# Optimization experiments

Measured on AMD Instinct MI355X. Metric: run time of the kernel, lower is better.

Reference implementation:

```python
import jax, jax.numpy as jnp
import numpy as np

HIDDEN = 512
HEADS = 8
LN_EPS = 1e-5


def setup_inputs() -> dict:
    key = jax.random.key(0)
    ks = jax.random.split(key, 10)
    n, bsz, h = 128, 4, HIDDEN
    state = jax.random.normal(ks[0], (n, n, bsz, h), dtype=jnp.float32)
    relation = jax.random.normal(ks[1], (n, n, bsz, h), dtype=jnp.float32)
    attn_mask = jnp.zeros((n, bsz, n), dtype=bool)  # key_padding_mask, True = pad
    std = 0.02
    Wq = jax.random.normal(ks[2], (h, h), dtype=jnp.float32) * std
    bq = jnp.zeros((h,), dtype=jnp.float32)
    Wk = jax.random.normal(ks[3], (h, h), dtype=jnp.float32) * std
    bk = jnp.zeros((h,), dtype=jnp.float32)
    Wp = jax.random.normal(ks[4], (h, 2 * h), dtype=jnp.float32) * std
    bp = jnp.zeros((h,), dtype=jnp.float32)
    gamma = jnp.ones((h,), dtype=jnp.float32)
    beta = jnp.zeros((h,), dtype=jnp.float32)
    return {"state": state, "relation": relation, "attn_mask": attn_mask, "n": n,
            "Wq": Wq, "bq": bq, "Wk": Wk, "bk": bk, "Wp": Wp, "bp": bp,
            "gamma": gamma, "beta": beta}


def reference(state, relation, attn_mask, n, Wq, bq, Wk, bk, Wp, bp, gamma, beta):
    # state, relation: [n, n, bsz, h]; attn_mask: [n, bsz, n] (True = pad key)
    h = state.shape[-1]
    dh = h // HEADS
    scale = dh ** -0.5
    # per-row self-attention weights (eval mode: attention dropout is identity)
    q = (jnp.einsum('itbh,oh->itbo', state, Wq) + bq) * scale
    k = jnp.einsum('isbh,oh->isbo', state, Wk) + bk
    qh = q.reshape(q.shape[0], q.shape[1], q.shape[2], HEADS, dh)
    kh = k.reshape(k.shape[0], k.shape[1], k.shape[2], HEADS, dh)
    scores = jnp.einsum('itbnd,isbnd->ibnts', qh, kh)  # [n, bsz, H, t, s]
    pad = attn_mask[:, :, None, None, :]               # [n, bsz, 1, 1, s]
    scores = jnp.where(pad, -jnp.inf, scores)
    probs = jax.nn.softmax(scores, axis=-1)
    w = probs.mean(axis=2)                             # avg over heads -> [n, bsz, t, s]
    # x[i,t,b] = sum_s w[i,b,t,s] * state[i,s,b]
    x = jnp.einsum('ibts,isbh->itbh', w, state)
    # rel_mix[i,t,b] = sum_s w[i,b,t,s] * relation[s,t,b]
    rel_mix = jnp.einsum('ibts,stbh->itbh', w, relation)
    cat = jnp.concatenate([x, rel_mix], axis=-1)       # [n, n, bsz, 2h]
    out = jax.nn.relu(jnp.einsum('itbc,hc->itbh', cat, Wp) + bp)
    # dropout is identity in eval mode; residual + layernorm
    y = state + out
    mu = y.mean(axis=-1, keepdims=True)
    var = y.var(axis=-1, keepdims=True)
    return gamma * (y - mu) * jax.lax.rsqrt(var + LN_EPS) + beta
```

## Files before the change

kernel.cpp:

```cpp
#include <hip/hip_runtime.h>

typedef unsigned short u16;
typedef __attribute__((ext_vector_type(4))) unsigned short u16x4;
typedef __attribute__((ext_vector_type(8))) unsigned short u16x8;
typedef __attribute__((ext_vector_type(8))) short bf16x8;
typedef __attribute__((ext_vector_type(4))) float f32x4;

__device__ __forceinline__ u16 f2bf(float f) {
  union { float f; unsigned u; } v; v.f = f;
  unsigned r = v.u + 0x7fffu + ((v.u >> 16) & 1u);
  return (u16)(r >> 16);
}
__device__ __forceinline__ float bf2f(u16 u) {
  union { unsigned u; float f; } v; v.u = ((unsigned)u) << 16;
  return v.f;
}
__device__ __forceinline__ u16x8 pack8(f32x4 a, f32x4 b) {
  u16x8 r = { f2bf(a.x), f2bf(a.y), f2bf(a.z), f2bf(a.w),
              f2bf(b.x), f2bf(b.y), f2bf(b.z), f2bf(b.w) };
  return r;
}
__device__ __forceinline__ void gload16(const void* g, void* l) {
  __builtin_amdgcn_global_load_lds(
      (const __attribute__((address_space(1))) unsigned int*)g,
      (__attribute__((address_space(3))) unsigned int*)l, 16, 0, 0);
}

__global__ __launch_bounds__(256) void k_prep(
    const float* __restrict__ Wq, const float* __restrict__ Wk,
    const float* __restrict__ bq, const float* __restrict__ bk,
    const float* __restrict__ Wp,
    u16* __restrict__ wqk, u16* __restrict__ wp, float* __restrict__ bqk) {
  int idx = blockIdx.x * 256 + threadIdx.x;
  if (idx < 524288) {
    int o = idx >> 9, hh = idx & 511;
    wqk[idx] = f2bf((o < 512) ? Wq[o * 512 + hh] * 0.125f : Wk[(o - 512) * 512 + hh]);
    wp[idx] = f2bf(Wp[idx]);
  }
  if (idx < 1024) bqk[idx] = (idx < 512) ? bq[idx] * 0.125f : bk[idx - 512];
}

__global__ __launch_bounds__(256) void k_cast(
    const float* __restrict__ src, u16* __restrict__ dst) {
  size_t idx = ((size_t)blockIdx.x * 256 + threadIdx.x) * 8;
  f32x4 v0 = *(const f32x4*)&src[idx];
  f32x4 v1 = *(const f32x4*)&src[idx + 4];
  *(u16x8*)&dst[idx] = pack8(v0, v1);
}

__global__ __launch_bounds__(256) void k_qkproj(
    const u16* __restrict__ stB, const u16* __restrict__ wqk,
    const float* __restrict__ bqk, u16* __restrict__ qk) {
  const int flat = blockIdx.x;
  const int xcd = flat & 7, local = flat >> 3;
  const int m0 = (xcd * 64 + (local >> 3)) * 128;
  const int n0 = (local & 7) * 128;
  __shared__ u16 smem[17408];
  u16* As = smem;
  u16* Bs = smem + 8192;
  const int tid = threadIdx.x, lane = tid & 63, wid = tid >> 6;
  const int l15 = lane & 15, l4 = lane >> 4;
  const int wm = (wid >> 1) * 64, wn = (wid & 1) * 64;
  const int lr = lane >> 3;
  const int lcs = ((lane & 7) ^ lr) * 8;
  const int s7 = l15 & 7;
  const f32x4 fz = {0.f, 0.f, 0.f, 0.f};
  f32x4 acc[4][4];
#pragma unroll
  for (int a = 0; a < 4; ++a)
#pragma unroll
    for (int c = 0; c < 4; ++c) acc[a][c] = fz;
  for (int k0 = 0; k0 < 512; k0 += 64) {
    if (k0) __syncthreads();
#pragma unroll
    for (int j = 0; j < 4; ++j) {
      int rb = wid * 32 + j * 8;
      gload16(&stB[(size_t)(m0 + rb + lr) * 512 + k0 + lcs], &As[rb * 64]);
      gload16(&wqk[(size_t)(n0 + rb + lr) * 512 + k0 + lcs], &Bs[rb * 64]);
    }
    __syncthreads();
#pragma unroll
    for (int kk = 0; kk < 64; kk += 32) {
      const int cshift = (((kk >> 3) + l4) ^ s7) * 8;
      bf16x8 af[4], bfr[4];
#pragma unroll
      for (int mf = 0; mf < 4; ++mf)
        af[mf] = *(const bf16x8*)&As[(wm + mf * 16 + l15) * 64 + cshift];
#pragma unroll
      for (int nf = 0; nf < 4; ++nf)
        bfr[nf] = *(const bf16x8*)&Bs[(wn + nf * 16 + l15) * 64 + cshift];
#pragma unroll
      for (int mf = 0; mf < 4; ++mf)
#pragma unroll
        for (int nf = 0; nf < 4; ++nf)
          acc[mf][nf] = __builtin_amdgcn_mfma_f32_16x16x32_bf16(af[mf], bfr[nf], acc[mf][nf], 0, 0, 0);
    }
  }
  float bias[4];
#pragma unroll
  for (int nf = 0; nf < 4; ++nf) bias[nf] = bqk[n0 + wn + nf * 16 + l15];
  __syncthreads();
  u16* Cs = smem;
#pragma unroll
  for (int mf = 0; mf < 4; ++mf)
#pragma unroll
    for (int nf = 0; nf < 4; ++nf)
#pragma unroll
      for (int r = 0; r < 4; ++r)
        Cs[(wm + mf * 16 + l4 * 4 + r) * 136 + wn + nf * 16 + l15] =
            f2bf(acc[mf][nf][r] + bias[nf]);
  __syncthreads();
#pragma unroll
  for (int rr = 0; rr < 8; ++rr) {
    int row = rr * 16 + (tid >> 4), c8 = (tid & 15) * 8;
    *(u16x8*)&qk[(size_t)(m0 + row) * 1024 + n0 + c8] = *(const u16x8*)&Cs[row * 136 + c8];
  }
}

__global__ __launch_bounds__(512) void k_scores(
    const u16* __restrict__ qk, const unsigned char* __restrict__ mask,
    u16* __restrict__ wbuf) {
  const int i = blockIdx.x, b = blockIdx.y;
  __shared__ u16 smem[2 * 128 * 72];
  u16* qs = smem;
  u16* ks = smem + 128 * 72;
  const int tid = threadIdx.x, lane = tid & 63, wid = tid >> 6;
  const int l15 = lane & 15, l4 = lane >> 4;
  float wacc[8][4];
#pragma unroll
  for (int nf = 0; nf < 8; ++nf)
#pragma unroll
    for (int r = 0; r < 4; ++r) wacc[nf][r] = 0.f;
  bool mk[8];
#pragma unroll
  for (int nf = 0; nf < 8; ++nf) mk[nf] = mask[i * 512 + b * 128 + nf * 16 + l15] != 0;
  const int arow = tid >> 3, acol = (tid & 7) * 8;
  const f32x4 fz = {0.f, 0.f, 0.f, 0.f};
  for (int h = 0; h < 8; ++h) {
    __syncthreads();
#pragma unroll
    for (int rr = 0; rr < 2; ++rr) {
      int row = rr * 64 + arow;
      int base = ((i * 128 + row) * 4 + b) * 1024 + h * 64 + acol;
      *(u16x8*)&qs[row * 72 + acol] = *(const u16x8*)&qk[base];
      *(u16x8*)&ks[row * 72 + acol] = *(const u16x8*)&qk[base + 512];
    }
    __syncthreads();
    f32x4 sc[8];
#pragma unroll
    for (int nf = 0; nf < 8; ++nf) sc[nf] = fz;
#pragma unroll
    for (int kk = 0; kk < 64; kk += 32) {
      bf16x8 a = *(const bf16x8*)&qs[(wid * 16 + l15) * 72 + kk + l4 * 8];
#pragma unroll
      for (int nf = 0; nf < 8; ++nf) {
        bf16x8 bb = *(const bf16x8*)&ks[(nf * 16 + l15) * 72 + kk + l4 * 8];
        sc[nf] = __builtin_amdgcn_mfma_f32_16x16x32_bf16(a, bb, sc[nf], 0, 0, 0);
      }
    }
#pragma unroll
    for (int r = 0; r < 4; ++r) {
      float mx = -3e38f;
#pragma unroll
      for (int nf = 0; nf < 8; ++nf) mx = fmaxf(mx, mk[nf] ? -3e38f : sc[nf][r]);
#pragma unroll
      for (int d = 1; d < 16; d <<= 1) mx = fmaxf(mx, __shfl_xor(mx, d, 64));
      float p[8], sum = 0.f;
#pragma unroll
      for (int nf = 0; nf < 8; ++nf) {
        p[nf] = mk[nf] ? 0.f : __expf(sc[nf][r] - mx);
        sum += p[nf];
      }
#pragma unroll
      for (int d = 1; d < 16; d <<= 1) sum += __shfl_xor(sum, d, 64);
      float inv = 0.125f / sum;
#pragma unroll
      for (int nf = 0; nf < 8; ++nf) wacc[nf][r] += p[nf] * inv;
    }
  }
#pragma unroll
  for (int nf = 0; nf < 8; ++nf)
#pragma unroll
    for (int r = 0; r < 4; ++r) {
      int t = wid * 16 + l4 * 4 + r;
      wbuf[((i * 4 + b) * 128 + t) * 128 + nf * 16 + l15] = f2bf(wacc[nf][r]);
    }
}

__global__ __launch_bounds__(256) void k_mix(
    const u16* __restrict__ stB, const float* __restrict__ relation,
    const u16* __restrict__ wbuf, u16* __restrict__ xbuf, u16* __restrict__ relbuf) {
  const int q = blockIdx.x, b = blockIdx.y;
  const int hc = blockIdx.z & 3, path = blockIdx.z >> 2;
  __shared__ u16 smem[2 * 128 * 136];
  u16* AT = smem;
  u16* WS = smem + 128 * 136;
  u16* T = WS;
  const int tid = threadIdx.x, lane = tid & 63, wid = tid >> 6;
  const int l15 = lane & 15, l4 = lane >> 4;
  const int wh = (wid >> 1) * 64, wc = (wid & 1) * 64;
  const int sr = tid >> 3, hseg = (tid & 7) * 16;
  const int th = tid >> 1, sseg = (tid & 1) * 16;
#pragma unroll
  for (int ch = 0; ch < 4; ++ch) {
    const int sbase = ch * 32;
    u16x8 r0, r1;
    if (path == 0) {
      size_t gaddr = ((size_t)(q * 128 + sbase + sr) * 4 + b) * 512 + hc * 128 + hseg;
      r0 = *(const u16x8*)&stB[gaddr];
      r1 = *(const u16x8*)&stB[gaddr + 8];
    } else {
      size_t gaddr = (((size_t)(sbase + sr) * 128 + q) * 4 + b) * 512 + hc * 128 + hseg;
      f32x4 v0 = *(const f32x4*)&relation[gaddr];
      f32x4 v1 = *(const f32x4*)&relation[gaddr + 4];
      f32x4 v2 = *(const f32x4*)&relation[gaddr + 8];
      f32x4 v3 = *(const f32x4*)&relation[gaddr + 12];
      r0 = pack8(v0, v1);
      r1 = pack8(v2, v3);
    }
    __syncthreads();
    *(u16x8*)&T[sr * 136 + hseg] = r0;
    *(u16x8*)&T[sr * 136 + hseg + 8] = r1;
    __syncthreads();
    u16x8 c0, c1;
#pragma unroll
    for (int j = 0; j < 8; ++j) c0[j] = T[(sseg + j) * 136 + th];
#pragma unroll
    for (int j = 0; j < 8; ++j) c1[j] = T[(sseg + 8 + j) * 136 + th];
    *(u16x8*)&AT[th * 136 + sbase + sseg] = c0;
    *(u16x8*)&AT[th * 136 + sbase + sseg + 8] = c1;
  }
  __syncthreads();
  const int r16 = tid >> 4, c8 = (tid & 15) * 8;
#pragma unroll
  for (int rr = 0; rr < 8; ++rr) {
    int row = rr * 16 + r16;
    const u16* src = (path == 0) ? &wbuf[((q * 4 + b) * 128 + row) * 128 + c8]
                                 : &wbuf[((row * 4 + b) * 128 + q) * 128 + c8];
    *(u16x8*)&WS[row * 136 + c8] = *(const u16x8*)src;
  }
  __syncthreads();
  const f32x4 fz = {0.f, 0.f, 0.f, 0.f};
  f32x4 acc[4][4];
#pragma unroll
  for (int a = 0; a < 4; ++a)
#pragma unroll
    for (int c = 0; c < 4; ++c) acc[a][c] = fz;
#pragma unroll
  for (int kk = 0; kk < 128; kk += 32) {
    bf16x8 af[4], bfr[4];
#pragma unroll
    for (int mf = 0; mf < 4; ++mf)
      af[mf] = *(const bf16x8*)&AT[(wh + mf * 16 + l15) * 136 + kk + l4 * 8];
#pragma unroll
    for (int nf = 0; nf < 4; ++nf)
      bfr[nf] = *(const bf16x8*)&WS[(wc + nf * 16 + l15) * 136 + kk + l4 * 8];
#pragma unroll
    for (int mf = 0; mf < 4; ++mf)
#pragma unroll
      for (int nf = 0; nf < 4; ++nf)
        acc[mf][nf] = __builtin_amdgcn_mfma_f32_16x16x32_bf16(af[mf], bfr[nf], acc[mf][nf], 0, 0, 0);
  }
  __syncthreads();
  u16* Cs = smem;
#pragma unroll
  for (int mf = 0; mf < 4; ++mf)
#pragma unroll
    for (int nf = 0; nf < 4; ++nf) {
      int h0 = wh + mf * 16 + l4 * 4;
      int oc = wc + nf * 16 + l15;
      u16x4 pk = { f2bf(acc[mf][nf][0]), f2bf(acc[mf][nf][1]),
                   f2bf(acc[mf][nf][2]), f2bf(acc[mf][nf][3]) };
      *(u16x4*)&Cs[oc * 136 + h0] = pk;
    }
  __syncthreads();
#pragma unroll
  for (int rr = 0; rr < 8; ++rr) {
    int o = rr * 16 + r16;
    u16x8 v = *(const u16x8*)&Cs[o * 136 + c8];
    if (path == 0)
      *(u16x8*)&xbuf[((q * 128 + o) * 4 + b) * 512 + hc * 128 + c8] = v;
    else
      *(u16x8*)&relbuf[((o * 128 + q) * 4 + b) * 512 + hc * 128 + c8] = v;
  }
}

__global__ __launch_bounds__(256) void k_proj(
    const u16* __restrict__ xbuf, const u16* __restrict__ relbuf,
    const u16* __restrict__ wp, const float* __restrict__ bp,
    u16* __restrict__ yb) {
  const int flat = blockIdx.x;
  const int xcd = flat & 7, local = flat >> 3;
  const int m0 = (xcd * 64 + (local >> 2)) * 128;
  const int n0 = (local & 3) * 128;
  __shared__ u16 smem[17408];
  u16* As = smem;
  u16* Bs = smem + 8192;
  const int tid = threadIdx.x, lane = tid & 63, wid = tid >> 6;
  const int l15 = lane & 15, l4 = lane >> 4;
  const int wm = (wid >> 1) * 64, wn = (wid & 1) * 64;
  const int lr = lane >> 3;
  const int lcs = ((lane & 7) ^ lr) * 8;
  const int s7 = l15 & 7;
  const f32x4 fz = {0.f, 0.f, 0.f, 0.f};
  f32x4 acc[4][4];
#pragma unroll
  for (int a = 0; a < 4; ++a)
#pragma unroll
    for (int c = 0; c < 4; ++c) acc[a][c] = fz;
  for (int k0 = 0; k0 < 1024; k0 += 64) {
    if (k0) __syncthreads();
    const u16* abase = (k0 < 512) ? xbuf + k0 : relbuf + (k0 - 512);
#pragma unroll
    for (int j = 0; j < 4; ++j) {
      int rb = wid * 32 + j * 8;
      gload16(&abase[(size_t)(m0 + rb + lr) * 512 + lcs], &As[rb * 64]);
      gload16(&wp[(size_t)(n0 + rb + lr) * 1024 + k0 + lcs], &Bs[rb * 64]);
    }
    __syncthreads();
#pragma unroll
    for (int kk = 0; kk < 64; kk += 32) {
      const int cshift = (((kk >> 3) + l4) ^ s7) * 8;
      bf16x8 af[4], bfr[4];
#pragma unroll
      for (int mf = 0; mf < 4; ++mf)
        af[mf] = *(const bf16x8*)&As[(wm + mf * 16 + l15) * 64 + cshift];
#pragma unroll
      for (int nf = 0; nf < 4; ++nf)
        bfr[nf] = *(const bf16x8*)&Bs[(wn + nf * 16 + l15) * 64 + cshift];
#pragma unroll
      for (int mf = 0; mf < 4; ++mf)
#pragma unroll
        for (int nf = 0; nf < 4; ++nf)
          acc[mf][nf] = __builtin_amdgcn_mfma_f32_16x16x32_bf16(af[mf], bfr[nf], acc[mf][nf], 0, 0, 0);
    }
  }
  float bias[4];
#pragma unroll
  for (int nf = 0; nf < 4; ++nf) bias[nf] = bp[n0 + wn + nf * 16 + l15];
  __syncthreads();
  u16* Cs = smem;
#pragma unroll
  for (int mf = 0; mf < 4; ++mf)
#pragma unroll
    for (int nf = 0; nf < 4; ++nf)
#pragma unroll
      for (int r = 0; r < 4; ++r)
        Cs[(wm + mf * 16 + l4 * 4 + r) * 136 + wn + nf * 16 + l15] =
            f2bf(fmaxf(acc[mf][nf][r] + bias[nf], 0.f));
  __syncthreads();
#pragma unroll
  for (int rr = 0; rr < 8; ++rr) {
    int row = rr * 16 + (tid >> 4), c8 = (tid & 15) * 8;
    *(u16x8*)&yb[(size_t)(m0 + row) * 512 + n0 + c8] = *(const u16x8*)&Cs[row * 136 + c8];
  }
}

__global__ __launch_bounds__(256) void k_ln(
    const u16* __restrict__ yb, const u16* __restrict__ stB,
    const float* __restrict__ gamma, const float* __restrict__ beta,
    float* __restrict__ out) {
  const int tid = threadIdx.x, lane = tid & 63, wid = tid >> 6;
  f32x4 g0 = *(const f32x4*)&gamma[lane * 8];
  f32x4 g1 = *(const f32x4*)&gamma[lane * 8 + 4];
  f32x4 be0 = *(const f32x4*)&beta[lane * 8];
  f32x4 be1 = *(const f32x4*)&beta[lane * 8 + 4];
  for (int row = blockIdx.x * 4 + wid; row < 65536; row += gridDim.x * 4) {
    size_t gbase = (size_t)row * 512 + lane * 8;
    u16x8 yv = *(const u16x8*)&yb[gbase];
    u16x8 sv = *(const u16x8*)&stB[gbase];
    float y[8];
#pragma unroll
    for (int j = 0; j < 8; ++j) y[j] = bf2f(yv[j]) + bf2f(sv[j]);
    float sum = 0.f, sq = 0.f;
#pragma unroll
    for (int j = 0; j < 8; ++j) { sum += y[j]; sq += y[j] * y[j]; }
#pragma unroll
    for (int d = 1; d < 64; d <<= 1) { sum += __shfl_xor(sum, d, 64); sq += __shfl_xor(sq, d, 64); }
    float mu = sum * (1.f / 512.f);
    float var = sq * (1.f / 512.f) - mu * mu;
    float rs = rsqrtf(var + 1e-5f);
    f32x4 o0, o1;
#pragma unroll
    for (int j = 0; j < 4; ++j) o0[j] = g0[j] * (y[j] - mu) * rs + be0[j];
#pragma unroll
    for (int j = 0; j < 4; ++j) o1[j] = g1[j] * (y[4 + j] - mu) * rs + be1[j];
    *(f32x4*)&out[gbase] = o0;
    *(f32x4*)&out[gbase + 4] = o1;
  }
}

extern "C" void kernel_launch(void* const* d_in, const int* in_sizes, int n_in,
                              void* d_out, int out_size, void* d_ws, size_t ws_size,
                              hipStream_t stream) {
  const float* state = (const float*)d_in[0];
  const float* relation = (const float*)d_in[1];
  const unsigned char* mask = (const unsigned char*)d_in[2];
  const float* Wq = (const float*)d_in[4];
  const float* bq = (const float*)d_in[5];
  const float* Wk = (const float*)d_in[6];
  const float* bk = (const float*)d_in[7];
  const float* Wp = (const float*)d_in[8];
  const float* bp = (const float*)d_in[9];
  const float* gamma = (const float*)d_in[10];
  const float* beta = (const float*)d_in[11];
  float* out = (float*)d_out;
  char* ws = (char*)d_ws;

  u16* qk     = (u16*)(ws);
  u16* xbuf   = (u16*)(ws);
  u16* relbuf = (u16*)(ws + 67108864);
  u16* yb     = (u16*)(ws + 134217728);
  u16* stB    = (u16*)(ws + 201326592);
  u16* wbuf   = (u16*)(ws + 268435456);
  u16* wqk    = (u16*)(ws + 285212672);
  u16* wp     = (u16*)(ws + 286261248);
  float* bqk  = (float*)(ws + 287309824);

  k_prep<<<2048, 256, 0, stream>>>(Wq, Wk, bq, bk, Wp, wqk, wp, bqk);
  k_cast<<<16384, 256, 0, stream>>>(state, stB);
  k_qkproj<<<4096, 256, 0, stream>>>(stB, wqk, bqk, qk);
  k_scores<<<dim3(128, 4), 512, 0, stream>>>(qk, mask, wbuf);
  k_mix<<<dim3(128, 4, 8), 256, 0, stream>>>(stB, relation, wbuf, xbuf, relbuf);
  k_proj<<<2048, 256, 0, stream>>>(xbuf, relbuf, wp, bp, yb);
  k_ln<<<2048, 256, 0, stream>>>(yb, stB, gamma, beta, out);
}
```

Baseline: 376.9 us.

## Fuse QK projection into per-row scores kernel to eliminate qk buffer

Merges the separate Q/K projection GEMM into the attention-scores kernel. Each (row i, batch b) block now computes the Q and K tiles for one head at a time from bf16 state and weights, writes them straight into shared memory, and then computes the scores. This removes writing the large bf16 qk intermediate to global memory and reading it back, plus one kernel launch. In exchange the projection runs with only 512 blocks and smaller per-wave tiles, with no double buffering, so GEMM efficiency and occupancy may drop.

New measurement: 415.1 us. 10.1% more time.

```diff
diff --git a/kernel.cpp b/kernel.cpp
--- a/kernel.cpp
+++ b/kernel.cpp
@@ -48,84 +48,22 @@
   *(u16x8*)&dst[idx] = pack8(v0, v1);
 }
 
-__global__ __launch_bounds__(256) void k_qkproj(
+__global__ __launch_bounds__(512) void k_qks(
     const u16* __restrict__ stB, const u16* __restrict__ wqk,
-    const float* __restrict__ bqk, u16* __restrict__ qk) {
-  const int flat = blockIdx.x;
-  const int xcd = flat & 7, local = flat >> 3;
-  const int m0 = (xcd * 64 + (local >> 3)) * 128;
-  const int n0 = (local & 7) * 128;
-  __shared__ u16 smem[17408];
-  u16* As = smem;
-  u16* Bs = smem + 8192;
+    const float* __restrict__ bqk, const unsigned char* __restrict__ mask,
+    u16* __restrict__ wbuf) {
+  const int i = blockIdx.x, b = blockIdx.y;
+  __shared__ u16 smem[18432];
+  u16* qs = smem;
+  u16* ks = smem + 9216;
+  u16* Ss = smem;
+  u16* Ws = smem + 8192;
   const int tid = threadIdx.x, lane = tid & 63, wid = tid >> 6;
   const int l15 = lane & 15, l4 = lane >> 4;
-  const int wm = (wid >> 1) * 64, wn = (wid & 1) * 64;
   const int lr = lane >> 3;
   const int lcs = ((lane & 7) ^ lr) * 8;
   const int s7 = l15 & 7;
-  const f32x4 fz = {0.f, 0.f, 0.f, 0.f};
-  f32x4 acc[4][4];
-#pragma unroll
-  for (int a = 0; a < 4; ++a)
-#pragma unroll
-    for (int c = 0; c < 4; ++c) acc[a][c] = fz;
-  for (int k0 = 0; k0 < 512; k0 += 64) {
-    if (k0) __syncthreads();
-#pragma unroll
-    for (int j = 0; j < 4; ++j) {
-      int rb = wid * 32 + j * 8;
-      gload16(&stB[(size_t)(m0 + rb + lr) * 512 + k0 + lcs], &As[rb * 64]);
-      gload16(&wqk[(size_t)(n0 + rb + lr) * 512 + k0 + lcs], &Bs[rb * 64]);
-    }
-    __syncthreads();
-#pragma unroll
-    for (int kk = 0; kk < 64; kk += 32) {
-      const int cshift = (((kk >> 3) + l4) ^ s7) * 8;
-      bf16x8 af[4], bfr[4];
-#pragma unroll
-      for (int mf = 0; mf < 4; ++mf)
-        af[mf] = *(const bf16x8*)&As[(wm + mf * 16 + l15) * 64 + cshift];
-#pragma unroll
-      for (int nf = 0; nf < 4; ++nf)
-        bfr[nf] = *(const bf16x8*)&Bs[(wn + nf * 16 + l15) * 64 + cshift];
-#pragma unroll
-      for (int mf = 0; mf < 4; ++mf)
-#pragma unroll
-        for (int nf = 0; nf < 4; ++nf)
-          acc[mf][nf] = __builtin_amdgcn_mfma_f32_16x16x32_bf16(af[mf], bfr[nf], acc[mf][nf], 0, 0, 0);
-    }
-  }
-  float bias[4];
-#pragma unroll
-  for (int nf = 0; nf < 4; ++nf) bias[nf] = bqk[n0 + wn + nf * 16 + l15];
-  __syncthreads();
-  u16* Cs = smem;
-#pragma unroll
-  for (int mf = 0; mf < 4; ++mf)
-#pragma unroll
-    for (int nf = 0; nf < 4; ++nf)
-#pragma unroll
-      for (int r = 0; r < 4; ++r)
-        Cs[(wm + mf * 16 + l4 * 4 + r) * 136 + wn + nf * 16 + l15] =
-            f2bf(acc[mf][nf][r] + bias[nf]);
-  __syncthreads();
-#pragma unroll
-  for (int rr = 0; rr < 8; ++rr) {
-    int row = rr * 16 + (tid >> 4), c8 = (tid & 15) * 8;
-    *(u16x8*)&qk[(size_t)(m0 + row) * 1024 + n0 + c8] = *(const u16x8*)&Cs[row * 136 + c8];
-  }
-}
-
-__global__ __launch_bounds__(512) void k_scores(
-    const u16* __restrict__ qk, const unsigned char* __restrict__ mask,
-    u16* __restrict__ wbuf) {
-  const int i = blockIdx.x, b = blockIdx.y;
-  __shared__ u16 smem[2 * 128 * 72];
-  u16* qs = smem;
-  u16* ks = smem + 128 * 72;
-  const int tid = threadIdx.x, lane = tid & 63, wid = tid >> 6;
-  const int l15 = lane & 15, l4 = lane >> 4;
+  const int wm = (wid >> 1) * 32, wn2 = (wid & 1) * 64;
   float wacc[8][4];
 #pragma unroll
   for (int nf = 0; nf < 8; ++nf)
@@ -134,17 +72,61 @@
   bool mk[8];
 #pragma unroll
   for (int nf = 0; nf < 8; ++nf) mk[nf] = mask[i * 512 + b * 128 + nf * 16 + l15] != 0;
-  const int arow = tid >> 3, acol = (tid & 7) * 8;
   const f32x4 fz = {0.f, 0.f, 0.f, 0.f};
+
   for (int h = 0; h < 8; ++h) {
+    f32x4 acc[2][4];
+#pragma unroll
+    for (int a = 0; a < 2; ++a)
+#pragma unroll
+      for (int c = 0; c < 4; ++c) acc[a][c] = fz;
+    for (int ks8 = 0; ks8 < 8; ++ks8) {
+      const int k0 = ks8 * 64;
+      __syncthreads();
+#pragma unroll
+      for (int j = 0; j < 2; ++j) {
+        int rb = wid * 16 + j * 8;
+        gload16(&stB[((size_t)(i * 128 + rb + lr) * 4 + b) * 512 + k0 + lcs], &Ss[rb * 64]);
+        const u16* wbase = (rb < 64) ? wqk + (size_t)(h * 64 + rb) * 512
+                                     : wqk + (size_t)(512 + h * 64 + (rb - 64)) * 512;
+        gload16(&wbase[(size_t)lr * 512 + k0 + lcs], &Ws[rb * 64]);
+      }
+      __syncthreads();
+#pragma unroll
+      for (int kk = 0; kk < 64; kk += 32) {
+        const int cshift = (((kk >> 3) + l4) ^ s7) * 8;
+        bf16x8 af[2], bfr[4];
+#pragma unroll
+        for (int mf = 0; mf < 2; ++mf)
+          af[mf] = *(const bf16x8*)&Ss[(wm + mf * 16 + l15) * 64 + cshift];
+#pragma unroll
+        for (int nf = 0; nf < 4; ++nf)
+          bfr[nf] = *(const bf16x8*)&Ws[(wn2 + nf * 16 + l15) * 64 + cshift];
+#pragma unroll
+        for (int mf = 0; mf < 2; ++mf)
+#pragma unroll
+          for (int nf = 0; nf < 4; ++nf)
+            acc[mf][nf] = __builtin_amdgcn_mfma_f32_16x16x32_bf16(af[mf], bfr[nf], acc[mf][nf], 0, 0, 0);
+      }
+    }
+    float bias[4];
+#pragma unroll
+    for (int nf = 0; nf < 4; ++nf)
+      bias[nf] = (wn2 == 0) ? bqk[h * 64 + nf * 16 + l15]
+                            : bqk[512 + h * 64 + nf * 16 + l15];
     __syncthreads();
 #pragma unroll
-    for (int rr = 0; rr < 2; ++rr) {
-      int row = rr * 64 + arow;
-      int base = ((i * 128 + row) * 4 + b) * 1024 + h * 64 + acol;
-      *(u16x8*)&qs[row * 72 + acol] = *(const u16x8*)&qk[base];
-      *(u16x8*)&ks[row * 72 + acol] = *(const u16x8*)&qk[base + 512];
-    }
+    for (int mf = 0; mf < 2; ++mf)
+#pragma unroll
+      for (int nf = 0; nf < 4; ++nf)
+#pragma unroll
+        for (int r = 0; r < 4; ++r) {
+          int row = wm + mf * 16 + l4 * 4 + r;
+          int col = wn2 + nf * 16 + l15;
+          u16 v = f2bf(acc[mf][nf][r] + bias[nf]);
+          if (wn2 == 0) qs[row * 72 + col] = v;
+          else ks[row * 72 + (col - 64)] = v;
+        }
     __syncthreads();
     f32x4 sc[8];
 #pragma unroll
@@ -407,7 +389,6 @@
   float* out = (float*)d_out;
   char* ws = (char*)d_ws;
 
-  u16* qk     = (u16*)(ws);
   u16* xbuf   = (u16*)(ws);
   u16* relbuf = (u16*)(ws + 67108864);
   u16* yb     = (u16*)(ws + 134217728);
@@ -419,8 +400,7 @@
 
   k_prep<<<2048, 256, 0, stream>>>(Wq, Wk, bq, bk, Wp, wqk, wp, bqk);
   k_cast<<<16384, 256, 0, stream>>>(state, stB);
-  k_qkproj<<<4096, 256, 0, stream>>>(stB, wqk, bqk, qk);
-  k_scores<<<dim3(128, 4), 512, 0, stream>>>(qk, mask, wbuf);
+  k_qks<<<dim3(128, 4), 512, 0, stream>>>(stB, wqk, bqk, mask, wbuf);
   k_mix<<<dim3(128, 4, 8), 256, 0, stream>>>(stB, relation, wbuf, xbuf, relbuf);
   k_proj<<<2048, 256, 0, stream>>>(xbuf, relbuf, wp, bp, yb);
   k_ln<<<2048, 256, 0, stream>>>(yb, stB, gamma, beta, out);
```
